# Kernel optimization log

Hardware: AMD Instinct MI355X
Metric: run time of the kernel (lower is better)

Reference implementation:

```python
import jax, jax.numpy as jnp
import numpy as np

B, S, V, D = 4, 128, 50257, 1024

def setup_inputs() -> dict:
    key = jax.random.key(0)
    k1, k2 = jax.random.split(key)
    # pred_probs: a probability simplex over vocab per (b, s); module initializes
    # to uniform by default, we use normalized uniform noise for a non-degenerate test.
    p = jax.random.uniform(k1, (B, S, V), dtype=jnp.float32) + 1e-3
    pred_probs = p / jnp.sum(p, axis=-1, keepdims=True)
    embed_weight = jax.random.normal(k2, (V, D), dtype=jnp.float32) * 0.02
    return {"pred_probs": pred_probs, "embed_weight": embed_weight}

def reference(pred_probs, embed_weight):
    # do_sample=False, st=False default path of TargetProbability.forward_multiple
    # predictions: argmax over vocab
    predictions = jnp.argmax(pred_probs, axis=-1)  # [B, S] int
    # soft embedding: (pred_probs.unsqueeze(-1) * embed_lut.weight).sum(-2)
    # == GEMM over the vocab dim, avoiding the [B,S,V,D] intermediate.
    pred_emb = jnp.einsum('bsv,vd->bsd', pred_probs, embed_weight)  # [B, S, D]
    return pred_emb, predictions, pred_probs
```

## Files before the change

kernel.cpp:

```cpp
#include <hip/hip_runtime.h>

#define MROWS 512
#define VDIM  50257
#define KP    50304
#define NDIM  1024
#define NST32 1572
#define KSPLIT 32
#define SC     50
#define PRED_OFF 524288
#define PP_OFF   524800
#define NPREP  4096
#define CHUNK  6284
#define NCONVW 12576

typedef unsigned short u16;
typedef unsigned int   u32;
typedef unsigned long long u64;
typedef __bf16 bf16x8 __attribute__((ext_vector_type(8)));
typedef float  f32x4  __attribute__((ext_vector_type(4)));
typedef float  f32x4u __attribute__((ext_vector_type(4), aligned(4)));

__device__ __forceinline__ u16 f2bf(float f) {
  u32 u = __float_as_uint(f);
  u32 r = (u + 0x7fffu + ((u >> 16) & 1u)) >> 16;
  return (u16)r;
}

__device__ __forceinline__ void gl_lds16(const u16* g, u16* l) {
  __builtin_amdgcn_global_load_lds(
      (const __attribute__((address_space(1))) u32*)(g),
      (__attribute__((address_space(3))) u32*)(l), 16, 0, 0);
}

__global__ __launch_bounds__(256) void prep_fused(const float* __restrict__ P,
                                                  const float* __restrict__ W,
                                                  float* __restrict__ out,
                                                  u16* __restrict__ A,
                                                  u16* __restrict__ BT,
                                                  u64* __restrict__ amax)
{
  const int tid = threadIdx.x;
  const int bx  = blockIdx.x;
  if (bx < NPREP) {
    const int m  = bx >> 3;
    const int c  = bx & 7;
    const int s0 = c * CHUNK;
    const int len = min(VDIM - s0, CHUNK);
    const float* row = P + (size_t)m * VDIM;
    float*       crw = out + PP_OFF + (size_t)m * VDIM;
    u16*        arow = A + (size_t)m * KP;

    if (tid < 32) { f32x4 z = {}; *(f32x4*)(out + (size_t)m * NDIM + c * 128 + tid * 4) = z; }

    u64 best = 0;
#define TRK(val, idx) do { \
      u64 pk = ((u64)__float_as_uint(val) << 32) | (u64)(0xFFFFu - (u32)(idx)); \
      best = best > pk ? best : pk; } while (0)

    const int nvec = len >> 2;
    int i = tid;
    for (; i + 256 < nvec; i += 512) {
      const int c0 = s0 + (i << 2);
      const int c1 = c0 + 1024;
      f32x4u v0 = *(const f32x4u*)(row + c0);
      f32x4u v1 = *(const f32x4u*)(row + c1);
      *(f32x4u*)(crw + c0) = v0;
      *(f32x4u*)(crw + c1) = v1;
      ushort4 o0, o1;
      o0.x = f2bf(v0[0]); o0.y = f2bf(v0[1]); o0.z = f2bf(v0[2]); o0.w = f2bf(v0[3]);
      o1.x = f2bf(v1[0]); o1.y = f2bf(v1[1]); o1.z = f2bf(v1[2]); o1.w = f2bf(v1[3]);
      *(ushort4*)(arow + c0) = o0;
      *(ushort4*)(arow + c1) = o1;
      TRK(v0[0], c0); TRK(v0[1], c0 + 1); TRK(v0[2], c0 + 2); TRK(v0[3], c0 + 3);
      TRK(v1[0], c1); TRK(v1[1], c1 + 1); TRK(v1[2], c1 + 2); TRK(v1[3], c1 + 3);
    }
    if (i < nvec) {
      const int c0 = s0 + (i << 2);
      f32x4u v = *(const f32x4u*)(row + c0);
      *(f32x4u*)(crw + c0) = v;
      ushort4 o;
      o.x = f2bf(v[0]); o.y = f2bf(v[1]); o.z = f2bf(v[2]); o.w = f2bf(v[3]);
      *(ushort4*)(arow + c0) = o;
      TRK(v[0], c0); TRK(v[1], c0 + 1); TRK(v[2], c0 + 2); TRK(v[3], c0 + 3);
    }
    if ((len & 3) && tid == 0) {
      const int col = s0 + (len & ~3);
      float v = row[col];
      crw[col] = v;
      arow[col] = f2bf(v);
      TRK(v, col);
    }
#undef TRK
    if (c == 7 && tid < KP - VDIM) arow[VDIM + tid] = 0;

    __shared__ u64 sb[256];
    sb[tid] = best;
    __syncthreads();
    for (int s = 128; s > 0; s >>= 1) {
      if (tid < s) { u64 o = sb[tid + s]; if (o > sb[tid]) sb[tid] = o; }
      __syncthreads();
    }
    if (tid == 0) atomicMax(&amax[m], sb[0]);
  } else {
    const int cidx = bx - NPREP;
    __shared__ u16 t[64][65];
    const int dt  = cidx & 15;
    const int vt  = cidx >> 4;
    const int v0  = vt << 6;
    const int d0  = dt << 6;
    const int c16 = tid & 15;
    const int r16 = tid >> 4;
#pragma unroll
    for (int p = 0; p < 4; ++p) {
      const int v  = v0 + p * 16 + r16;
      const int vl = p * 16 + r16;
      float4 w = make_float4(0.f, 0.f, 0.f, 0.f);
      if (v < VDIM) w = *(const float4*)(W + (size_t)v * NDIM + d0 + c16 * 4);
      t[c16 * 4 + 0][vl] = f2bf(w.x);
      t[c16 * 4 + 1][vl] = f2bf(w.y);
      t[c16 * 4 + 2][vl] = f2bf(w.z);
      t[c16 * 4 + 3][vl] = f2bf(w.w);
    }
    __syncthreads();
#pragma unroll
    for (int p = 0; p < 4; ++p) {
      const int dl = p * 16 + r16;
      const int vl = c16 * 4;
      ushort4 o;
      o.x = t[dl][vl]; o.y = t[dl][vl + 1]; o.z = t[dl][vl + 2]; o.w = t[dl][vl + 3];
      *(ushort4*)(BT + (size_t)(d0 + dl) * KP + v0 + vl) = o;
    }
  }
}

__global__ __launch_bounds__(512, 1) void gemm_kernel(const u16* __restrict__ A,
                                                      const u16* __restrict__ BT,
                                                      const u64* __restrict__ amax,
                                                      float* __restrict__ out)
{
  __shared__ u16 ldsA[4][256 * 32];
  __shared__ u16 ldsB[4][256 * 32];

  const int bx  = blockIdx.x;
  const int kc  = (bx & 7) | ((bx >> 6) << 3);
  const int mn  = (bx >> 3) & 7;
  const int m0  = (mn & 1) << 8;
  const int n0  = (mn >> 1) << 8;
  const int ks0 = kc * SC;
  const int ks1 = min(NST32, ks0 + SC);
  const int tid  = threadIdx.x;
  const int wid  = tid >> 6;
  const int lane = tid & 63;
  const int wr   = wid >> 2;
  const int wc   = wid & 3;

  if (bx == 0) {
    u64 p = amax[tid];
    out[PRED_OFF + tid] = (float)(0xFFFF - (int)(p & 0xFFFFu));
  }

  const int srow4 = lane >> 2;
  const int gk    = ((lane & 3) ^ (srow4 & 3)) << 3;
  const u16* gA = A  + (size_t)(m0 + wid * 32 + srow4) * KP + gk;
  const u16* gB = BT + (size_t)(n0 + wid * 32 + srow4) * KP + gk;

  f32x4 acc[8][4] = {};

  const int r   = lane & 15;
  const int q4  = lane >> 4;
  const int s0r = ((q4 ^ (r & 3)) << 3);
  const int rbA = (wr * 128 + r) * 32;
  const int rbB = (wc * 64 + r) * 32;

#define STAGE(buf, ks) do {                                           \
    const size_t k_ = (size_t)(ks) << 5;                              \
    gl_lds16(gA + k_,                 &ldsA[buf][(wid * 32) * 32]);   \
    gl_lds16(gA + k_ + (size_t)16*KP, &ldsA[buf][(wid * 32 + 16) * 32]); \
    gl_lds16(gB + k_,                 &ldsB[buf][(wid * 32) * 32]);   \
    gl_lds16(gB + k_ + (size_t)16*KP, &ldsB[buf][(wid * 32 + 16) * 32]); \
  } while (0)

  STAGE(0, ks0);
  if (ks0 + 1 < ks1) STAGE(1, ks0 + 1);
  if (ks0 + 2 < ks1) STAGE(2, ks0 + 2);

  int b = 0;
  for (int ks = ks0; ks < ks1; ++ks) {
    if (ks + 2 < ks1)      asm volatile("s_waitcnt vmcnt(8) lgkmcnt(0)" ::: "memory");
    else if (ks + 1 < ks1) asm volatile("s_waitcnt vmcnt(4) lgkmcnt(0)" ::: "memory");
    else                   asm volatile("s_waitcnt vmcnt(0) lgkmcnt(0)" ::: "memory");
    __builtin_amdgcn_s_barrier();
    if (ks + 3 < ks1) STAGE((b + 3) & 3, ks + 3);

    const u16* lA = ldsA[b];
    const u16* lB = ldsB[b];
    bf16x8 av[8], bv[4];
#pragma unroll
    for (int i = 0; i < 8; ++i) av[i] = *(const bf16x8*)(lA + rbA + i * 16 * 32 + s0r);
#pragma unroll
    for (int j = 0; j < 4; ++j) bv[j] = *(const bf16x8*)(lB + rbB + j * 16 * 32 + s0r);

    __builtin_amdgcn_s_setprio(1);
#pragma unroll
    for (int i = 0; i < 8; ++i)
#pragma unroll
      for (int j = 0; j < 4; ++j)
        acc[i][j] = __builtin_amdgcn_mfma_f32_16x16x32_bf16(av[i], bv[j], acc[i][j], 0, 0, 0);
    __builtin_amdgcn_s_setprio(0);
    __builtin_amdgcn_sched_barrier(0);
    b = (b + 1) & 3;
  }
#undef STAGE

  const int col = lane & 15;
  const int r4  = q4 << 2;
#pragma unroll
  for (int i = 0; i < 8; ++i)
#pragma unroll
    for (int j = 0; j < 4; ++j)
#pragma unroll
      for (int rr = 0; rr < 4; ++rr) {
        const int mm = m0 + wr * 128 + i * 16 + r4 + rr;
        const int nn = n0 + wc * 64 + j * 16 + col;
        atomicAdd(out + (size_t)mm * NDIM + nn, acc[i][j][rr]);
      }
}

extern "C" void kernel_launch(void* const* d_in, const int* in_sizes, int n_in,
                              void* d_out, int out_size, void* d_ws, size_t ws_size,
                              hipStream_t stream) {
  const float* P = (const float*)d_in[0];
  const float* W = (const float*)d_in[1];
  float* out = (float*)d_out;
  u64* amax = (u64*)d_ws;
  u16* A  = (u16*)((char*)d_ws + 4096);
  u16* BT = A + (size_t)MROWS * KP;

  hipMemsetAsync(amax, 0, MROWS * sizeof(u64), stream);
  prep_fused<<<NPREP + NCONVW, 256, 0, stream>>>(P, W, out, A, BT, amax);
  gemm_kernel<<<256, 512, 0, stream>>>(A, BT, amax, out);
}
```

Baseline: 237.0 us.

## Split GEMM k-step into two MFMA halves with interleaved staging and new LDS swizzle

```diff
diff --git a/kernel.cpp b/kernel.cpp
--- a/kernel.cpp
+++ b/kernel.cpp
@@ -6,17 +6,18 @@
 #define NDIM  1024
 #define NST32 1572
 #define KSPLIT 32
-#define SC     50
+#define SC     25
 #define PRED_OFF 524288
 #define PP_OFF   524800
 #define NPREP  4096
-#define CHUNK  6284
+#define CHUNK  6288
 #define NCONVW 12576
 
 typedef unsigned short u16;
 typedef unsigned int   u32;
 typedef unsigned long long u64;
 typedef __bf16 bf16x8 __attribute__((ext_vector_type(8)));
+typedef u16    u16x8  __attribute__((ext_vector_type(8)));
 typedef float  f32x4  __attribute__((ext_vector_type(4)));
 typedef float  f32x4u __attribute__((ext_vector_type(4), aligned(4)));
 
@@ -56,40 +57,36 @@
 #define TRK(val, idx) do { \
       u64 pk = ((u64)__float_as_uint(val) << 32) | (u64)(0xFFFFu - (u32)(idx)); \
       best = best > pk ? best : pk; } while (0)
-
-    const int nvec = len >> 2;
+#define GRP(cc) do {                                                     \
+      f32x4u va = *(const f32x4u*)(row + (cc));                          \
+      f32x4u vb = *(const f32x4u*)(row + (cc) + 4);                      \
+      *(f32x4u*)(crw + (cc))     = va;                                   \
+      *(f32x4u*)(crw + (cc) + 4) = vb;                                   \
+      u16x8 o;                                                           \
+      o[0]=f2bf(va[0]); o[1]=f2bf(va[1]); o[2]=f2bf(va[2]); o[3]=f2bf(va[3]); \
+      o[4]=f2bf(vb[0]); o[5]=f2bf(vb[1]); o[6]=f2bf(vb[2]); o[7]=f2bf(vb[3]); \
+      *(u16x8*)(arow + (cc)) = o;                                        \
+      TRK(va[0],(cc)); TRK(va[1],(cc)+1); TRK(va[2],(cc)+2); TRK(va[3],(cc)+3); \
+      TRK(vb[0],(cc)+4); TRK(vb[1],(cc)+5); TRK(vb[2],(cc)+6); TRK(vb[3],(cc)+7); \
+    } while (0)
+
+    const int ng = len >> 3;
     int i = tid;
-    for (; i + 256 < nvec; i += 512) {
-      const int c0 = s0 + (i << 2);
-      const int c1 = c0 + 1024;
-      f32x4u v0 = *(const f32x4u*)(row + c0);
-      f32x4u v1 = *(const f32x4u*)(row + c1);
-      *(f32x4u*)(crw + c0) = v0;
-      *(f32x4u*)(crw + c1) = v1;
-      ushort4 o0, o1;
-      o0.x = f2bf(v0[0]); o0.y = f2bf(v0[1]); o0.z = f2bf(v0[2]); o0.w = f2bf(v0[3]);
-      o1.x = f2bf(v1[0]); o1.y = f2bf(v1[1]); o1.z = f2bf(v1[2]); o1.w = f2bf(v1[3]);
-      *(ushort4*)(arow + c0) = o0;
-      *(ushort4*)(arow + c1) = o1;
-      TRK(v0[0], c0); TRK(v0[1], c0 + 1); TRK(v0[2], c0 + 2); TRK(v0[3], c0 + 3);
-      TRK(v1[0], c1); TRK(v1[1], c1 + 1); TRK(v1[2], c1 + 2); TRK(v1[3], c1 + 3);
-    }
-    if (i < nvec) {
-      const int c0 = s0 + (i << 2);
-      f32x4u v = *(const f32x4u*)(row + c0);
-      *(f32x4u*)(crw + c0) = v;
-      ushort4 o;
-      o.x = f2bf(v[0]); o.y = f2bf(v[1]); o.z = f2bf(v[2]); o.w = f2bf(v[3]);
-      *(ushort4*)(arow + c0) = o;
-      TRK(v[0], c0); TRK(v[1], c0 + 1); TRK(v[2], c0 + 2); TRK(v[3], c0 + 3);
-    }
-    if ((len & 3) && tid == 0) {
-      const int col = s0 + (len & ~3);
+    for (; i + 256 < ng; i += 512) {
+      const int c0 = s0 + (i << 3);
+      const int c1 = c0 + 2048;
+      GRP(c0);
+      GRP(c1);
+    }
+    if (i < ng) GRP(s0 + (i << 3));
+    if (tid < (len & 7)) {
+      const int col = s0 + (ng << 3) + tid;
       float v = row[col];
       crw[col] = v;
       arow[col] = f2bf(v);
       TRK(v, col);
     }
+#undef GRP
 #undef TRK
     if (c == 7 && tid < KP - VDIM) arow[VDIM + tid] = 0;
 
@@ -146,8 +143,8 @@
   const int mn  = (bx >> 3) & 7;
   const int m0  = (mn & 1) << 8;
   const int n0  = (mn >> 1) << 8;
-  const int ks0 = kc * SC;
-  const int ks1 = min(NST32, ks0 + SC);
+  const int ks0 = kc * SC * 2;
+  const int ks1 = min(NST32, ks0 + SC * 2);
   const int tid  = threadIdx.x;
   const int wid  = tid >> 6;
   const int lane = tid & 63;
@@ -159,58 +156,85 @@
     out[PRED_OFF + tid] = (float)(0xFFFF - (int)(p & 0xFFFFu));
   }
 
-  const int srow4 = lane >> 2;
-  const int gk    = ((lane & 3) ^ (srow4 & 3)) << 3;
-  const u16* gA = A  + (size_t)(m0 + wid * 32 + srow4) * KP + gk;
-  const u16* gB = BT + (size_t)(n0 + wid * 32 + srow4) * KP + gk;
+  const int sp  = lane >> 3;
+  const int sx  = (lane & 7) ^ sp;
+  const int srow = 2 * sp + (sx >> 2);
+  const int skel = (sx & 3) << 3;
+  const u16* gA = A  + (size_t)(m0 + wid * 32 + srow) * KP + skel;
+  const u16* gB = BT + (size_t)(n0 + wid * 32 + srow) * KP + skel;
 
   f32x4 acc[8][4] = {};
 
   const int r   = lane & 15;
   const int q4  = lane >> 4;
-  const int s0r = ((q4 ^ (r & 3)) << 3);
-  const int rbA = (wr * 128 + r) * 32;
-  const int rbB = (wc * 64 + r) * 32;
-
-#define STAGE(buf, ks) do {                                           \
-    const size_t k_ = (size_t)(ks) << 5;                              \
-    gl_lds16(gA + k_,                 &ldsA[buf][(wid * 32) * 32]);   \
+  const int sl  = (((r & 1) << 2) | q4) ^ ((r >> 1) & 7);
+  const int rb2A = (wr * 128 + (r & ~1)) * 32 + sl * 8;
+  const int rb2B = (wc * 64  + (r & ~1)) * 32 + sl * 8;
+
+#define STAGE_A(buf, ks) do {                                            \
+    const size_t k_ = (size_t)(ks) << 5;                                 \
+    gl_lds16(gA + k_,                 &ldsA[buf][(wid * 32) * 32]);      \
     gl_lds16(gA + k_ + (size_t)16*KP, &ldsA[buf][(wid * 32 + 16) * 32]); \
-    gl_lds16(gB + k_,                 &ldsB[buf][(wid * 32) * 32]);   \
+  } while (0)
+#define STAGE_B(buf, ks) do {                                            \
+    const size_t k_ = (size_t)(ks) << 5;                                 \
+    gl_lds16(gB + k_,                 &ldsB[buf][(wid * 32) * 32]);      \
     gl_lds16(gB + k_ + (size_t)16*KP, &ldsB[buf][(wid * 32 + 16) * 32]); \
   } while (0)
 
-  STAGE(0, ks0);
-  if (ks0 + 1 < ks1) STAGE(1, ks0 + 1);
-  if (ks0 + 2 < ks1) STAGE(2, ks0 + 2);
+  STAGE_A(0, ks0); STAGE_B(0, ks0);
+  if (ks0 + 1 < ks1) { STAGE_A(1, ks0 + 1); STAGE_B(1, ks0 + 1); }
+  if (ks0 + 2 < ks1) { STAGE_A(2, ks0 + 2); STAGE_B(2, ks0 + 2); }
+  if (ks0 + 2 < ks1)      asm volatile("s_waitcnt vmcnt(8)" ::: "memory");
+  else if (ks0 + 1 < ks1) asm volatile("s_waitcnt vmcnt(4)" ::: "memory");
+  else                    asm volatile("s_waitcnt vmcnt(0)" ::: "memory");
+  __builtin_amdgcn_s_barrier();
 
   int b = 0;
   for (int ks = ks0; ks < ks1; ++ks) {
-    if (ks + 2 < ks1)      asm volatile("s_waitcnt vmcnt(8) lgkmcnt(0)" ::: "memory");
-    else if (ks + 1 < ks1) asm volatile("s_waitcnt vmcnt(4) lgkmcnt(0)" ::: "memory");
-    else                   asm volatile("s_waitcnt vmcnt(0) lgkmcnt(0)" ::: "memory");
-    __builtin_amdgcn_s_barrier();
-    if (ks + 3 < ks1) STAGE((b + 3) & 3, ks + 3);
-
     const u16* lA = ldsA[b];
     const u16* lB = ldsB[b];
-    bf16x8 av[8], bv[4];
-#pragma unroll
-    for (int i = 0; i < 8; ++i) av[i] = *(const bf16x8*)(lA + rbA + i * 16 * 32 + s0r);
-#pragma unroll
-    for (int j = 0; j < 4; ++j) bv[j] = *(const bf16x8*)(lB + rbB + j * 16 * 32 + s0r);
-
+
+    bf16x8 av[4], bv[4];
+#pragma unroll
+    for (int i = 0; i < 4; ++i) av[i] = *(const bf16x8*)(lA + rb2A + i * 512);
+#pragma unroll
+    for (int j = 0; j < 4; ++j) bv[j] = *(const bf16x8*)(lB + rb2B + j * 512);
+    if (ks + 3 < ks1) STAGE_A((b + 3) & 3, ks + 3);
+    __builtin_amdgcn_s_barrier();
+    asm volatile("s_waitcnt lgkmcnt(0)" ::: "memory");
+    __builtin_amdgcn_sched_barrier(0);
     __builtin_amdgcn_s_setprio(1);
 #pragma unroll
-    for (int i = 0; i < 8; ++i)
+    for (int i = 0; i < 4; ++i)
 #pragma unroll
       for (int j = 0; j < 4; ++j)
         acc[i][j] = __builtin_amdgcn_mfma_f32_16x16x32_bf16(av[i], bv[j], acc[i][j], 0, 0, 0);
     __builtin_amdgcn_s_setprio(0);
+    __builtin_amdgcn_s_barrier();
+
+    bf16x8 aw[4];
+#pragma unroll
+    for (int i = 0; i < 4; ++i) aw[i] = *(const bf16x8*)(lA + rb2A + (i + 4) * 512);
+    if (ks + 3 < ks1) STAGE_B((b + 3) & 3, ks + 3);
+    __builtin_amdgcn_s_barrier();
+    asm volatile("s_waitcnt lgkmcnt(0)" ::: "memory");
     __builtin_amdgcn_sched_barrier(0);
+    __builtin_amdgcn_s_setprio(1);
+#pragma unroll
+    for (int i = 0; i < 4; ++i)
+#pragma unroll
+      for (int j = 0; j < 4; ++j)
+        acc[i + 4][j] = __builtin_amdgcn_mfma_f32_16x16x32_bf16(aw[i], bv[j], acc[i + 4][j], 0, 0, 0);
+    __builtin_amdgcn_s_setprio(0);
+    if (ks + 3 < ks1)      asm volatile("s_waitcnt vmcnt(8)" ::: "memory");
+    else if (ks + 2 < ks1) asm volatile("s_waitcnt vmcnt(4)" ::: "memory");
+    else if (ks + 1 < ks1) asm volatile("s_waitcnt vmcnt(0)" ::: "memory");
+    __builtin_amdgcn_s_barrier();
     b = (b + 1) & 3;
   }
-#undef STAGE
+#undef STAGE_A
+#undef STAGE_B
 
   const int col = lane & 15;
   const int r4  = q4 << 2;
```

Result: faster. 223.6 us (-5.6%).
